# Performance work log

Measured on AMD Instinct MI355X. Metric: run time of the kernel, lower is better.

The kernel has to match this reference:

```python
import jax, jax.numpy as jnp
import numpy as np

USR_NUM = 100000
D_IN = 32
D_HID = 32
D_MID = 16
D_OUT = 2
N_EDGES = 1600000
EPS = 1e-16  # matches torch_geometric.utils.softmax denominator eps


def _glorot(key, shape):
    fan_in, fan_out = shape[0], shape[1]
    lim = np.sqrt(6.0 / (fan_in + fan_out))
    return jax.random.uniform(key, shape, jnp.float32, -lim, lim)


def setup_inputs() -> dict:
    key = jax.random.key(0)
    ks = jax.random.split(key, 16)
    inp = {
        "edge_index": jax.random.randint(ks[0], (2, N_EDGES), 0, USR_NUM, dtype=jnp.int64)
        if jax.config.jax_enable_x64 else jax.random.randint(ks[0], (2, N_EDGES), 0, USR_NUM).astype(jnp.int32),
        "emb": jax.random.normal(ks[1], (USR_NUM, D_IN), jnp.float32),
        # conv1: TransformerConv(32 -> 32, heads=1)
        "Wq1": _glorot(ks[2], (D_IN, D_HID)), "bq1": jnp.zeros((D_HID,), jnp.float32),
        "Wk1": _glorot(ks[3], (D_IN, D_HID)), "bk1": jnp.zeros((D_HID,), jnp.float32),
        "Wv1": _glorot(ks[4], (D_IN, D_HID)), "bv1": jnp.zeros((D_HID,), jnp.float32),
        "Ws1": _glorot(ks[5], (D_IN, D_HID)), "bs1": jnp.zeros((D_HID,), jnp.float32),
        # conv2: TransformerConv(32 -> 16, heads=1)
        "Wq2": _glorot(ks[6], (D_HID, D_MID)), "bq2": jnp.zeros((D_MID,), jnp.float32),
        "Wk2": _glorot(ks[7], (D_HID, D_MID)), "bk2": jnp.zeros((D_MID,), jnp.float32),
        "Wv2": _glorot(ks[8], (D_HID, D_MID)), "bv2": jnp.zeros((D_MID,), jnp.float32),
        "Ws2": _glorot(ks[9], (D_HID, D_MID)), "bs2": jnp.zeros((D_MID,), jnp.float32),
        # output: Linear(16 -> 2)
        "Wo": _glorot(ks[10], (D_MID, D_OUT)), "bo": jnp.zeros((D_OUT,), jnp.float32),
    }
    return inp


def transformer_conv(x, src, dst, Wq, bq, Wk, bk, Wv, bv, Ws, bs, n_nodes):
    # edge (j=src -> i=dst): alpha_ij = softmax_i( <q_i, k_j> / sqrt(d) )
    d = Wq.shape[1]
    q = (x @ Wq + bq)[dst]          # [E, d]
    k = (x @ Wk + bk)[src]          # [E, d]
    v = (x @ Wv + bv)[src]          # [E, d]
    alpha = jnp.sum(q * k, axis=-1) / jnp.sqrt(jnp.float32(d))  # [E]
    # segment softmax over incoming edges of each destination node
    seg_max = jax.ops.segment_max(alpha, dst, num_segments=n_nodes)  # [N]
    e = jnp.exp(alpha - seg_max[dst])
    seg_sum = jax.ops.segment_sum(e, dst, num_segments=n_nodes)      # [N]
    w = e / (seg_sum[dst] + EPS)
    agg = jax.ops.segment_sum(v * w[:, None], dst, num_segments=n_nodes)  # [N, d]
    return agg + x @ Ws + bs  # root/skip connection (PyG default root_weight=True)


def reference(edge_index, emb,
              Wq1, bq1, Wk1, bk1, Wv1, bv1, Ws1, bs1,
              Wq2, bq2, Wk2, bk2, Wv2, bv2, Ws2, bs2,
              Wo, bo):
    src, dst = edge_index[0], edge_index[1]
    h = transformer_conv(emb, src, dst, Wq1, bq1, Wk1, bk1, Wv1, bv1, Ws1, bs1, USR_NUM)
    h = jax.nn.relu(h)
    h = transformer_conv(h, src, dst, Wq2, bq2, Wk2, bk2, Wv2, bv2, Ws2, bs2, USR_NUM)
    h = jax.nn.relu(h)
    return h @ Wo + bo  # [N, 2]
```

## Files before the change

### kernel.cpp

```cpp
#include <hip/hip_runtime.h>
#include <hip/hip_bf16.h>

typedef __hip_bfloat16 bf16;
typedef unsigned int uint;
typedef unsigned short ushort;

#define N_NODES 100000
#define N_EDGES_C 1600000
#define NSB 196
#define NSBP 200
#define SBCAP 10240
#define RND 2048
#define EPB (RND / 256)
#define NBIN 64
#define G_RAD ((N_EDGES_C + RND - 1) / RND)
#define NHB 392
#define HCAP 5632
#define NSLOT (NHB * 256)
#define NCHUNK 16
#define KEYN (256 * NCHUNK)

__device__ __forceinline__ float ldf(const void* p, long i, int isbf) {
    return isbf ? __bfloat162float(((const bf16*)p)[i]) : ((const float*)p)[i];
}
__device__ __forceinline__ int ldidx(const int* ei, long pos, int is64) {
    return is64 ? ei[2 * pos] : ei[pos];
}
__device__ __forceinline__ ushort bfb(float x) {
    bf16 h = __float2bfloat16(x);
    return *(ushort*)&h;
}
__device__ __forceinline__ float bl(uint u) { return __uint_as_float(u << 16); }
__device__ __forceinline__ float bh(uint u) { return __uint_as_float(u & 0xFFFF0000u); }

__global__ void setup_kernel(
    const void* emb, const int* ei,
    const void* Wq1, const void* bq1, const void* Wk1, const void* bk1,
    const void* Wv1, const void* bv1, const void* Ws1, const void* bs1,
    const void* Wq2, const void* bq2, const void* Wk2, const void* bk2,
    const void* Wv2, const void* bv2, const void* Ws2, const void* bs2,
    const void* Wo, const void* bo,
    int* flags, float* wp1, float* bp1, float* wp2, float* bp2, float* woF,
    int* curSB) {
    __shared__ int sf0;
    int t = threadIdx.x;
    if (t < 64) {
        const bf16* pb = (const bf16*)emb;
        int bad = 0;
        for (int i = t; i < 256; i += 64) {
            float v = __bfloat162float(pb[i]);
            if (!(v > -1.0e6f && v < 1.0e6f)) bad++;
        }
        int nz = 0;
        for (int i = 2 * t + 1; i < 256; i += 128) nz += (ei[i] != 0) ? 1 : 0;
#pragma unroll
        for (int m = 32; m >= 1; m >>= 1) {
            bad += __shfl_xor(bad, m, 64);
            nz  += __shfl_xor(nz, m, 64);
        }
        if (t == 0) {
            int f0 = (bad <= 8) ? 1 : 0;
            flags[0] = f0;
            flags[1] = (nz == 0) ? 1 : 0;
            sf0 = f0;
        }
    }
    __syncthreads();
    int isbf = sf0;
    for (int i = t; i < 1024; i += 256) {
        wp1[i]        = ldf(Wq1, i, isbf);
        wp1[1024 + i] = ldf(Wk1, i, isbf);
        wp1[2048 + i] = ldf(Wv1, i, isbf);
        wp1[3072 + i] = ldf(Ws1, i, isbf);
    }
    for (int i = t; i < 512; i += 256) {
        wp2[i]        = ldf(Wq2, i, isbf);
        wp2[512 + i]  = ldf(Wk2, i, isbf);
        wp2[1024 + i] = ldf(Wv2, i, isbf);
        wp2[1536 + i] = ldf(Ws2, i, isbf);
    }
    if (t < 32) {
        bp1[t] = ldf(bq1, t, isbf); bp1[32 + t] = ldf(bk1, t, isbf);
        bp1[64 + t] = ldf(bv1, t, isbf); bp1[96 + t] = ldf(bs1, t, isbf);
        woF[t] = ldf(Wo, t, isbf);
    }
    if (t < 16) {
        bp2[t] = ldf(bq2, t, isbf); bp2[16 + t] = ldf(bk2, t, isbf);
        bp2[32 + t] = ldf(bv2, t, isbf); bp2[48 + t] = ldf(bs2, t, isbf);
    }
    if (t < 2) woF[32 + t] = ldf(bo, t, isbf);
    curSB[t] = 0;
}

template <int DOUT, bool RUNTIME_DTYPE>
__device__ __forceinline__ void node_linear_body(
    const void* __restrict__ X, const float* __restrict__ wpack,
    const float* __restrict__ bpack, const int* __restrict__ flags,
    float* __restrict__ q, ushort* __restrict__ kvb, float* __restrict__ s,
    int bid, float* __restrict__ sW, float* __restrict__ sbias, float* __restrict__ sX) {
    const int TPN = DOUT / 4;
    const int NPB = 256 / TPN;
    const int W_ELEMS = 4 * 32 * DOUT;

    const float4* wp4 = (const float4*)wpack;
    float4* sW4 = (float4*)sW;
    for (int i = threadIdx.x; i < W_ELEMS / 4; i += 256) sW4[i] = wp4[i];
    if (threadIdx.x < 4 * DOUT) sbias[threadIdx.x] = bpack[threadIdx.x];
    const int base = bid * NPB * 32;
    bool useBf = RUNTIME_DTYPE && (flags[0] != 0);
    if (useBf) {
        for (int i = threadIdx.x; i < NPB * 32; i += 256) {
            int g = base + i;
            float xv = (g < N_NODES * 32) ? __bfloat162float(((const bf16*)X)[g]) : 0.0f;
            sX[(i >> 5) * 36 + (i & 31)] = xv;
        }
    } else {
        for (int i = threadIdx.x; i < NPB * 32; i += 256) {
            int g = base + i;
            sX[(i >> 5) * 36 + (i & 31)] = (g < N_NODES * 32) ? ((const float*)X)[g] : 0.0f;
        }
    }
    __syncthreads();

    int l = threadIdx.x / TPN;
    int c4 = (threadIdx.x % TPN) * 4;
    int n = bid * NPB + l;
    if (n >= N_NODES) return;

    float xr[32];
#pragma unroll
    for (int j = 0; j < 8; j++) {
        float4 t4 = *(const float4*)&sX[l * 36 + 4 * j];
        xr[4 * j] = t4.x; xr[4 * j + 1] = t4.y; xr[4 * j + 2] = t4.z; xr[4 * j + 3] = t4.w;
    }
    float acc[4][4];
#pragma unroll
    for (int m = 0; m < 4; m++)
#pragma unroll
        for (int j = 0; j < 4; j++) acc[m][j] = sbias[m * DOUT + c4 + j];

#pragma unroll
    for (int t = 0; t < 32; t++) {
#pragma unroll
        for (int m = 0; m < 4; m++) {
            float4 w = *(const float4*)&sW[(m * 32 + t) * DOUT + c4];
            acc[m][0] += xr[t] * w.x;
            acc[m][1] += xr[t] * w.y;
            acc[m][2] += xr[t] * w.z;
            acc[m][3] += xr[t] * w.w;
        }
    }
    size_t o = (size_t)n * DOUT + c4;
    *(float4*)&q[o] = make_float4(acc[0][0], acc[0][1], acc[0][2], acc[0][3]);
    *(float4*)&s[o] = make_float4(acc[3][0], acc[3][1], acc[3][2], acc[3][3]);
    size_t okv = (size_t)n * 2 * DOUT + c4;
    ushort4 kp = make_ushort4(bfb(acc[1][0]), bfb(acc[1][1]), bfb(acc[1][2]), bfb(acc[1][3]));
    ushort4 vp = make_ushort4(bfb(acc[2][0]), bfb(acc[2][1]), bfb(acc[2][2]), bfb(acc[2][3]));
    *(ushort4*)&kvb[okv]        = kp;
    *(ushort4*)&kvb[okv + DOUT] = vp;
}

struct RadixS {
    int cnt[256]; int excl[256]; int gbase[NSBP];
    uint sVal[RND]; unsigned char sSb[RND];
};
struct LinS { float sW[4096]; float sbias[128]; float sX[32 * 36]; };
union alignas(16) FusedS { RadixS r; LinS l; };

__global__ void __launch_bounds__(256, 4) fused_ra_nl(
    const int* __restrict__ ei, const int* __restrict__ flags,
    int* __restrict__ curSB, uint* __restrict__ pairsSB,
    const void* __restrict__ X, const float* __restrict__ wpack,
    const float* __restrict__ bpack,
    float* __restrict__ q, ushort* __restrict__ kvb, float* __restrict__ s) {
    __shared__ FusedS u;
    if (blockIdx.x >= G_RAD) {
        node_linear_body<32, true>(X, wpack, bpack, flags, q, kvb, s,
                                   (int)blockIdx.x - G_RAD, u.l.sW, u.l.sbias, u.l.sX);
        return;
    }
    int* cnt = u.r.cnt; int* excl = u.r.excl; int* gbase = u.r.gbase;
    uint* sVal = u.r.sVal; unsigned char* sSb = u.r.sSb;
    const int is64 = flags[1];
    int t = threadIdx.x;
    cnt[t] = 0;
    __syncthreads();
    long base = (long)blockIdx.x * RND;

    int mySb[EPB]; int myRank[EPB]; uint myPk[EPB];
#pragma unroll
    for (int r = 0; r < EPB; r++) {
        long e = base + r * 256 + t;
        mySb[r] = -1;
        if (e < N_EDGES_C) {
            int d = ldidx(ei, (long)N_EDGES_C + e, is64);
            int src = ldidx(ei, e, is64);
            int sb = d >> 9;
            myPk[r] = (uint)src | ((uint)(d & 511) << 17);
            myRank[r] = atomicAdd(&cnt[sb], 1);
            mySb[r] = sb;
        }
    }
    __syncthreads();
    int v = cnt[t];
    excl[t] = v;
    __syncthreads();
    for (int off = 1; off < 256; off <<= 1) {
        int u2 = (t >= off) ? excl[t - off] : 0;
        __syncthreads();
        excl[t] += u2;
        __syncthreads();
    }
    int myExcl = excl[t] - v;
    __syncthreads();
    excl[t] = myExcl;
    __syncthreads();
#pragma unroll
    for (int r = 0; r < EPB; r++) {
        if (mySb[r] >= 0) {
            int pos = excl[mySb[r]] + myRank[r];
            sVal[pos] = myPk[r];
            sSb[pos] = (unsigned char)mySb[r];
        }
    }
    __syncthreads();
    if (t < NSBP)
        gbase[t] = (cnt[t] > 0) ? atomicAdd(&curSB[t], cnt[t]) : 0;
    __syncthreads();
    int tot = excl[NSBP - 1] + cnt[NSBP - 1];
    for (int i = t; i < tot; i += 256) {
        int sb = sSb[i];
        int gp = gbase[sb] + (i - excl[sb]);
        if (gp < SBCAP)
            pairsSB[(size_t)sb * SBCAP + gp] = sVal[i];
    }
}

__global__ void __launch_bounds__(256, 2) radix_b(
    const int* __restrict__ curSB, const uint* __restrict__ pairsSB,
    int* __restrict__ esrc,
    int* __restrict__ rowbeg, int* __restrict__ rowend,
    int* __restrict__ perm) {
    __shared__ uint sP[HCAP];
    __shared__ int dcnt[KEYN];
    __shared__ int dexcl[KEYN];
    __shared__ int dcur[KEYN];
    __shared__ int part[256];
    __shared__ int hbin[NBIN], hbase[NBIN], hcur[NBIN];
    __shared__ int scnt;
    int sbh = blockIdx.x;
    int parent = sbh >> 1, half = sbh & 1;
    int t = threadIdx.x;
    int n = min(curSB[parent], SBCAP);
    for (int i = t; i < KEYN; i += 256) { dcnt[i] = 0; dcur[i] = 0; }
    if (t < NBIN) { hbin[t] = 0; hcur[t] = 0; }
    if (t == 0) scnt = 0;
    perm[sbh * 256 + t] = -1;
    __syncthreads();
    const uint* srcp = pairsSB + (size_t)parent * SBCAP;
    for (int i = t; i < n; i += 256) {
        uint pk = srcp[i];
        if (((pk >> 25) & 1u) == (uint)half) {
            int m = atomicAdd(&scnt, 1);
            if (m < HCAP) sP[m] = pk;
            int key = (int)((pk >> 17) & 255) * NCHUNK + (int)((pk & 0x1FFFFu) >> 13);
            atomicAdd(&dcnt[key], 1);
        }
    }
    __syncthreads();
    int nc = min(scnt, HCAP);
    const int kb = t * NCHUNK;
    int sum = 0;
#pragma unroll
    for (int j = 0; j < NCHUNK; j++) sum += dcnt[kb + j];
    int v = sum;
    part[t] = v;
    __syncthreads();
    for (int off = 1; off < 256; off <<= 1) {
        int u2 = (t >= off) ? part[t - off] : 0;
        __syncthreads();
        part[t] += u2;
        __syncthreads();
    }
    int run = part[t] - v;
    int myExcl = run;
#pragma unroll
    for (int j = 0; j < NCHUNK; j++) { dexcl[kb + j] = run; run += dcnt[kb + j]; }
    __syncthreads();
    const int EB = sbh * HCAP;
    int dst = sbh * 256 + t;
    int mybin = -1;
    if (dst < N_NODES) {
        rowbeg[dst] = EB + min(myExcl, HCAP);
        rowend[dst] = EB + min(myExcl + v, HCAP);
        mybin = min(v, NBIN - 1);
        atomicAdd(&hbin[mybin], 1);
    }
    __syncthreads();
    if (t < 64) {
        int hv = hbin[t];
        int sfx = hv;
#pragma unroll
        for (int off = 1; off < 64; off <<= 1) {
            int u2 = __shfl_down(sfx, off, 64);
            if (t + off < 64) sfx += u2;
        }
        hbase[t] = sfx - hv;
    }
    __syncthreads();
    if (dst < N_NODES) {
        int r = atomicAdd(&hcur[mybin], 1);
        perm[sbh * 256 + hbase[mybin] + r] = dst;
    }
    for (int i = t; i < nc; i += 256) {
        uint pk = sP[i];
        int key = (int)((pk >> 17) & 255) * NCHUNK + (int)((pk & 0x1FFFFu) >> 13);
        int p2 = dexcl[key] + atomicAdd(&dcur[key], 1);
        if (p2 < HCAP) esrc[EB + p2] = (int)(pk & 0x1FFFF);
    }
}

template <int D, bool LAYER2>
__global__ void gather_attn(const int* __restrict__ perm,
                            const int* __restrict__ rowbeg, const int* __restrict__ rowend,
                            const int* __restrict__ esrc,
                            const float* __restrict__ q, const ushort* __restrict__ kvb,
                            const float* __restrict__ s,
                            const float* __restrict__ wp2,
                            const float* __restrict__ bp2,
                            const float* __restrict__ woF,
                            const int* __restrict__ flags,
                            float* __restrict__ q2o, ushort* __restrict__ kvb2o,
                            float* __restrict__ s2o,
                            void* __restrict__ out) {
    const int LPD = D / 8;
    const int G = 64 / LPD;
    __shared__ float sW2[2048];
    __shared__ float sb2[64];
    __shared__ float sH[64 * 36];
    __shared__ int sDst[64];

    if constexpr (!LAYER2) {
        for (int i = threadIdx.x; i < 2048; i += 256) sW2[i] = wp2[i];
        if (threadIdx.x < 64) sb2[threadIdx.x] = bp2[threadIdx.x];
    }

    int lane = threadIdx.x & 63;
    int wave = (blockIdx.x * blockDim.x + threadIdx.x) >> 6;
    int g = lane / LPD;
    int c = lane % LPD;
    int idx = wave * G + g;
    if constexpr (LAYER2) {
        if (idx >= NSLOT) return;
    }
    int dst = perm[idx];
    if constexpr (LAYER2) {
        if (dst < 0) return;
    }
    bool alive = (dst >= 0);

    const float rsq = (D == 32) ? 0.17677669529663689f : 0.25f;
    float4 qa = make_float4(0.f, 0.f, 0.f, 0.f), qb = qa;
    int beg = 0, end = 0;
    if (alive) {
        qa = *(const float4*)(q + (size_t)dst * D + 8 * c);
        qb = *(const float4*)(q + (size_t)dst * D + 8 * c + 4);
        beg = rowbeg[dst]; end = rowend[dst];
    }

    const char* kvbase = (const char*)kvb;
    const int ROW = 4 * D;
    const int koff = 16 * c;
    const int voff = 2 * D + 16 * c;

    float sum0 = 0.f, sum1 = 0.f;
    float a0[8] = {0,0,0,0,0,0,0,0};
    float a1[8] = {0,0,0,0,0,0,0,0};

    uint4 kq[4], vq[4];
#pragma unroll
    for (int r = 0; r < 4; r++) {
        int sn = (beg + r < end) ? esrc[beg + r] : 0;
        const char* p = kvbase + (size_t)sn * ROW;
        kq[r] = *(const uint4*)(p + koff);
        vq[r] = *(const uint4*)(p + voff);
    }

    for (int e = beg; e < end; e += 4) {
        uint4 kc[4], vc[4];
#pragma unroll
        for (int r = 0; r < 4; r++) { kc[r] = kq[r]; vc[r] = vq[r]; }
#pragma unroll
        for (int r = 0; r < 4; r++) {
            if (e + 4 + r < end) {
                const char* p = kvbase + (size_t)esrc[e + 4 + r] * ROW;
                kq[r] = *(const uint4*)(p + koff);
                vq[r] = *(const uint4*)(p + voff);
            }
        }
#pragma unroll
        for (int r = 0; r < 4; r++) {
            if (e + r < end) {
                uint4 kA = kc[r], vA = vc[r];
                float pd = qa.x * bl(kA.x) + qa.y * bh(kA.x) + qa.z * bl(kA.y) + qa.w * bh(kA.y)
                         + qb.x * bl(kA.z) + qb.y * bh(kA.z) + qb.z * bl(kA.w) + qb.w * bh(kA.w);
#pragma unroll
                for (int m = LPD / 2; m >= 1; m >>= 1) pd += __shfl_xor(pd, m, LPD);
                float ex = __expf(fminf(fmaxf(pd * rsq, -80.0f), 80.0f));
                if (r & 1) {
                    sum1 += ex;
                    a1[0] += bl(vA.x) * ex; a1[1] += bh(vA.x) * ex;
                    a1[2] += bl(vA.y) * ex; a1[3] += bh(vA.y) * ex;
                    a1[4] += bl(vA.z) * ex; a1[5] += bh(vA.z) * ex;
                    a1[6] += bl(vA.w) * ex; a1[7] += bh(vA.w) * ex;
                } else {
                    sum0 += ex;
                    a0[0] += bl(vA.x) * ex; a0[1] += bh(vA.x) * ex;
                    a0[2] += bl(vA.y) * ex; a0[3] += bh(vA.y) * ex;
                    a0[4] += bl(vA.z) * ex; a0[5] += bh(vA.z) * ex;
                    a0[6] += bl(vA.w) * ex; a0[7] += bh(vA.w) * ex;
                }
            }
        }
    }
    float inv = 1.0f / (sum0 + sum1 + 1e-16f);
    float4 sa = make_float4(0.f, 0.f, 0.f, 0.f), sbv = sa;
    if (alive) {
        sa  = *(const float4*)(s + (size_t)dst * D + 8 * c);
        sbv = *(const float4*)(s + (size_t)dst * D + 8 * c + 4);
    }
    float h[8];
    h[0] = (a0[0] + a1[0]) * inv + sa.x;  h[1] = (a0[1] + a1[1]) * inv + sa.y;
    h[2] = (a0[2] + a1[2]) * inv + sa.z;  h[3] = (a0[3] + a1[3]) * inv + sa.w;
    h[4] = (a0[4] + a1[4]) * inv + sbv.x; h[5] = (a0[5] + a1[5]) * inv + sbv.y;
    h[6] = (a0[6] + a1[6]) * inv + sbv.z; h[7] = (a0[7] + a1[7]) * inv + sbv.w;
#pragma unroll
    for (int j = 0; j < 8; j++) h[j] = h[j] > 0.0f ? h[j] : 0.0f;

    if constexpr (!LAYER2) {
        int gl = (threadIdx.x >> 6) * G + g;
        if (alive) {
            *(float4*)&sH[gl * 36 + 8 * c]     = make_float4(h[0], h[1], h[2], h[3]);
            *(float4*)&sH[gl * 36 + 8 * c + 4] = make_float4(h[4], h[5], h[6], h[7]);
        }
        if (c == 0) sDst[gl] = dst;
        __syncthreads();
        int l = threadIdx.x >> 2;
        int c4 = (threadIdx.x & 3) * 4;
        int nd = sDst[l];
        if (nd >= 0) {
            float acc2[4][4];
#pragma unroll
            for (int m = 0; m < 4; m++)
#pragma unroll
                for (int j = 0; j < 4; j++) acc2[m][j] = sb2[m * 16 + c4 + j];
#pragma unroll
            for (int t2 = 0; t2 < 32; t2++) {
                float xv = sH[l * 36 + t2];
#pragma unroll
                for (int m = 0; m < 4; m++) {
                    float4 w = *(const float4*)&sW2[(m * 32 + t2) * 16 + c4];
                    acc2[m][0] += xv * w.x;
                    acc2[m][1] += xv * w.y;
                    acc2[m][2] += xv * w.z;
                    acc2[m][3] += xv * w.w;
                }
            }
            size_t o = (size_t)nd * 16 + c4;
            *(float4*)&q2o[o] = make_float4(acc2[0][0], acc2[0][1], acc2[0][2], acc2[0][3]);
            *(float4*)&s2o[o] = make_float4(acc2[3][0], acc2[3][1], acc2[3][2], acc2[3][3]);
            size_t okv = (size_t)nd * 32 + c4;
            ushort4 kp = make_ushort4(bfb(acc2[1][0]), bfb(acc2[1][1]), bfb(acc2[1][2]), bfb(acc2[1][3]));
            ushort4 vp = make_ushort4(bfb(acc2[2][0]), bfb(acc2[2][1]), bfb(acc2[2][2]), bfb(acc2[2][3]));
            *(ushort4*)&kvb2o[okv]      = kp;
            *(ushort4*)&kvb2o[okv + 16] = vp;
        }
    } else {
        float p0 = 0.f, p1 = 0.f;
#pragma unroll
        for (int j = 0; j < 8; j++) {
            p0 += h[j] * woF[(8 * c + j) * 2 + 0];
            p1 += h[j] * woF[(8 * c + j) * 2 + 1];
        }
#pragma unroll
        for (int m = LPD / 2; m >= 1; m >>= 1) {
            p0 += __shfl_xor(p0, m, LPD);
            p1 += __shfl_xor(p1, m, LPD);
        }
        if (c == 0) {
            float o0 = p0 + woF[32];
            float o1 = p1 + woF[33];
            if (flags[0]) {
                ((bf16*)out)[dst * 2 + 0] = __float2bfloat16(o0);
                ((bf16*)out)[dst * 2 + 1] = __float2bfloat16(o1);
            } else {
                ((float*)out)[dst * 2 + 0] = o0;
                ((float*)out)[dst * 2 + 1] = o1;
            }
        }
    }
}

extern "C" void kernel_launch(void* const* d_in, const int* in_sizes, int n_in,
                              void* d_out, int out_size, void* d_ws, size_t ws_size,
                              hipStream_t stream) {
    const int* ei  = (const int*)d_in[0];
    const void* emb = d_in[1];
    const void *Wq1 = d_in[2],  *bq1 = d_in[3];
    const void *Wk1 = d_in[4],  *bk1 = d_in[5];
    const void *Wv1 = d_in[6],  *bv1 = d_in[7];
    const void *Ws1 = d_in[8],  *bs1 = d_in[9];
    const void *Wq2 = d_in[10], *bq2 = d_in[11];
    const void *Wk2 = d_in[12], *bk2 = d_in[13];
    const void *Wv2 = d_in[14], *bv2 = d_in[15];
    const void *Ws2 = d_in[16], *bs2 = d_in[17];
    const void *Wo  = d_in[18], *bo  = d_in[19];

    const size_t ND   = (size_t)N_NODES * 32;
    const size_t ND16 = (size_t)N_NODES * 16;
    const size_t SBTOT = (size_t)NSB * SBCAP;
    const size_t ESRC_TOT = (size_t)NHB * HCAP;
    float* base   = (float*)d_ws;
    int*   flags  = (int*)base;
    float* wp1    = base + 64;
    float* bp1    = wp1 + 4096;
    float* wp2    = bp1 + 128;
    float* bp2    = wp2 + 2048;
    float* woF    = bp2 + 64;
    int*   curSB  = (int*)(woF + 64);
    int*   rowbeg = curSB + 256;
    int*   rowend = rowbeg + N_NODES;
    int*   perm   = rowend + N_NODES;
    float* p      = (float*)(perm + NSLOT);
    float* q      = p; p += ND;
    float* s      = p; p += ND;
    ushort* kvb   = (ushort*)p; p += ND;
    float* q2     = p; p += ND16;
    float* s2     = p; p += ND16;
    ushort* kvb2  = (ushort*)p; p += ND16;
    int*   esrc   = (int*)p; p += ESRC_TOT;
    uint*  pairsSB = (uint*)p;

    const int B = 256;
    const int gNL32  = (N_NODES + 31) / 32;
    const int gFused = G_RAD + gNL32;
    const int gG1    = NSLOT / 64;
    const int gG2    = NSLOT / 128;

    setup_kernel<<<1, B, 0, stream>>>(emb, ei,
        Wq1, bq1, Wk1, bk1, Wv1, bv1, Ws1, bs1,
        Wq2, bq2, Wk2, bk2, Wv2, bv2, Ws2, bs2, Wo, bo,
        flags, wp1, bp1, wp2, bp2, woF, curSB);

    fused_ra_nl<<<gFused, B, 0, stream>>>(ei, flags, curSB, pairsSB,
                                          emb, wp1, bp1, q, kvb, s);

    radix_b<<<NHB, B, 0, stream>>>(curSB, pairsSB, esrc, rowbeg, rowend, perm);

    gather_attn<32, false><<<gG1, B, 0, stream>>>(
        perm, rowbeg, rowend, esrc, q, kvb, s, wp2, bp2, nullptr, flags,
        q2, kvb2, s2, nullptr);

    gather_attn<16, true><<<gG2, B, 0, stream>>>(
        perm, rowbeg, rowend, esrc, q2, kvb2, s2, nullptr, nullptr, woF, flags,
        nullptr, nullptr, nullptr, d_out);
}
```

Baseline: 265.0 us.

## Bucket edges directly into 256-node superbuckets and permute gather wave order

Result: no change. 260.7 us (-1.6%).

```diff
diff --git a/kernel.cpp b/kernel.cpp
--- a/kernel.cpp
+++ b/kernel.cpp
@@ -7,16 +7,14 @@
 
 #define N_NODES 100000
 #define N_EDGES_C 1600000
-#define NSB 196
-#define NSBP 200
-#define SBCAP 10240
+#define NSB2 392
+#define NSB2P 512
 #define RND 2048
 #define EPB (RND / 256)
 #define NBIN 64
 #define G_RAD ((N_EDGES_C + RND - 1) / RND)
-#define NHB 392
 #define HCAP 5632
-#define NSLOT (NHB * 256)
+#define NSLOT (NSB2 * 256)
 #define NCHUNK 16
 #define KEYN (256 * NCHUNK)
 
@@ -89,7 +87,7 @@
         bp2[32 + t] = ldf(bv2, t, isbf); bp2[48 + t] = ldf(bs2, t, isbf);
     }
     if (t < 2) woF[32 + t] = ldf(bo, t, isbf);
-    curSB[t] = 0;
+    curSB[t] = 0; curSB[t + 256] = 0;
 }
 
 template <int DOUT, bool RUNTIME_DTYPE>
@@ -161,8 +159,8 @@
 }
 
 struct RadixS {
-    int cnt[256]; int excl[256]; int gbase[NSBP];
-    uint sVal[RND]; unsigned char sSb[RND];
+    int cnt[NSB2P]; int excl[NSB2P]; int part[256]; int gbase[NSB2P];
+    uint sVal[RND]; ushort sSb[RND];
 };
 struct LinS { float sW[4096]; float sbias[128]; float sX[32 * 36]; };
 union alignas(16) FusedS { RadixS r; LinS l; };
@@ -179,11 +177,11 @@
                                    (int)blockIdx.x - G_RAD, u.l.sW, u.l.sbias, u.l.sX);
         return;
     }
-    int* cnt = u.r.cnt; int* excl = u.r.excl; int* gbase = u.r.gbase;
-    uint* sVal = u.r.sVal; unsigned char* sSb = u.r.sSb;
+    int* cnt = u.r.cnt; int* excl = u.r.excl; int* part = u.r.part; int* gbase = u.r.gbase;
+    uint* sVal = u.r.sVal; ushort* sSb = u.r.sSb;
     const int is64 = flags[1];
     int t = threadIdx.x;
-    cnt[t] = 0;
+    cnt[t] = 0; cnt[t + 256] = 0;
     __syncthreads();
     long base = (long)blockIdx.x * RND;
 
@@ -195,44 +193,44 @@
         if (e < N_EDGES_C) {
             int d = ldidx(ei, (long)N_EDGES_C + e, is64);
             int src = ldidx(ei, e, is64);
-            int sb = d >> 9;
-            myPk[r] = (uint)src | ((uint)(d & 511) << 17);
+            int sb = d >> 8;
+            myPk[r] = (uint)src | ((uint)(d & 255) << 17);
             myRank[r] = atomicAdd(&cnt[sb], 1);
             mySb[r] = sb;
         }
     }
     __syncthreads();
-    int v = cnt[t];
-    excl[t] = v;
+    int v0 = cnt[2 * t], v1 = cnt[2 * t + 1];
+    int sum2 = v0 + v1;
+    part[t] = sum2;
     __syncthreads();
     for (int off = 1; off < 256; off <<= 1) {
-        int u2 = (t >= off) ? excl[t - off] : 0;
+        int u2 = (t >= off) ? part[t - off] : 0;
         __syncthreads();
-        excl[t] += u2;
+        part[t] += u2;
         __syncthreads();
     }
-    int myExcl = excl[t] - v;
-    __syncthreads();
-    excl[t] = myExcl;
+    int basex = part[t] - sum2;
+    excl[2 * t]     = basex;
+    excl[2 * t + 1] = basex + v0;
     __syncthreads();
 #pragma unroll
     for (int r = 0; r < EPB; r++) {
         if (mySb[r] >= 0) {
             int pos = excl[mySb[r]] + myRank[r];
             sVal[pos] = myPk[r];
-            sSb[pos] = (unsigned char)mySb[r];
-        }
-    }
-    __syncthreads();
-    if (t < NSBP)
-        gbase[t] = (cnt[t] > 0) ? atomicAdd(&curSB[t], cnt[t]) : 0;
-    __syncthreads();
-    int tot = excl[NSBP - 1] + cnt[NSBP - 1];
+            sSb[pos] = (ushort)mySb[r];
+        }
+    }
+    for (int i = t; i < NSB2P; i += 256)
+        gbase[i] = (cnt[i] > 0) ? atomicAdd(&curSB[i], cnt[i]) : 0;
+    __syncthreads();
+    int tot = excl[NSB2P - 1] + cnt[NSB2P - 1];
     for (int i = t; i < tot; i += 256) {
         int sb = sSb[i];
         int gp = gbase[sb] + (i - excl[sb]);
-        if (gp < SBCAP)
-            pairsSB[(size_t)sb * SBCAP + gp] = sVal[i];
+        if (gp < HCAP)
+            pairsSB[(size_t)sb * HCAP + gp] = sVal[i];
     }
 }
 
@@ -247,28 +245,21 @@
     __shared__ int dcur[KEYN];
     __shared__ int part[256];
     __shared__ int hbin[NBIN], hbase[NBIN], hcur[NBIN];
-    __shared__ int scnt;
     int sbh = blockIdx.x;
-    int parent = sbh >> 1, half = sbh & 1;
     int t = threadIdx.x;
-    int n = min(curSB[parent], SBCAP);
+    int n = min(curSB[sbh], HCAP);
     for (int i = t; i < KEYN; i += 256) { dcnt[i] = 0; dcur[i] = 0; }
     if (t < NBIN) { hbin[t] = 0; hcur[t] = 0; }
-    if (t == 0) scnt = 0;
     perm[sbh * 256 + t] = -1;
     __syncthreads();
-    const uint* srcp = pairsSB + (size_t)parent * SBCAP;
+    const uint* srcp = pairsSB + (size_t)sbh * HCAP;
     for (int i = t; i < n; i += 256) {
         uint pk = srcp[i];
-        if (((pk >> 25) & 1u) == (uint)half) {
-            int m = atomicAdd(&scnt, 1);
-            if (m < HCAP) sP[m] = pk;
-            int key = (int)((pk >> 17) & 255) * NCHUNK + (int)((pk & 0x1FFFFu) >> 13);
-            atomicAdd(&dcnt[key], 1);
-        }
-    }
-    __syncthreads();
-    int nc = min(scnt, HCAP);
+        sP[i] = pk;
+        int key = (int)((pk >> 17) & 255) * NCHUNK + (int)((pk & 0x1FFFFu) >> 13);
+        atomicAdd(&dcnt[key], 1);
+    }
+    __syncthreads();
     const int kb = t * NCHUNK;
     int sum = 0;
 #pragma unroll
@@ -312,7 +303,7 @@
         int r = atomicAdd(&hcur[mybin], 1);
         perm[sbh * 256 + hbase[mybin] + r] = dst;
     }
-    for (int i = t; i < nc; i += 256) {
+    for (int i = t; i < n; i += 256) {
         uint pk = sP[i];
         int key = (int)((pk >> 17) & 255) * NCHUNK + (int)((pk & 0x1FFFFu) >> 13);
         int p2 = dexcl[key] + atomicAdd(&dcur[key], 1);
@@ -335,6 +326,7 @@
                             void* __restrict__ out) {
     const int LPD = D / 8;
     const int G = 64 / LPD;
+    const int WPC = 256 / G;
     __shared__ float sW2[2048];
     __shared__ float sb2[64];
     __shared__ float sH[64 * 36];
@@ -346,13 +338,12 @@
     }
 
     int lane = threadIdx.x & 63;
-    int wave = (blockIdx.x * blockDim.x + threadIdx.x) >> 6;
+    int W = (blockIdx.x * blockDim.x + threadIdx.x) >> 6;
     int g = lane / LPD;
     int c = lane % LPD;
-    int idx = wave * G + g;
-    if constexpr (LAYER2) {
-        if (idx >= NSLOT) return;
-    }
+    int chunkc = W / WPC;
+    int window = ((W % WPC) * 5) % WPC;
+    int idx = chunkc * 256 + window * G + g;
     int dst = perm[idx];
     if constexpr (LAYER2) {
         if (dst < 0) return;
@@ -518,8 +509,7 @@
 
     const size_t ND   = (size_t)N_NODES * 32;
     const size_t ND16 = (size_t)N_NODES * 16;
-    const size_t SBTOT = (size_t)NSB * SBCAP;
-    const size_t ESRC_TOT = (size_t)NHB * HCAP;
+    const size_t SBTOT = (size_t)NSB2 * HCAP;
     float* base   = (float*)d_ws;
     int*   flags  = (int*)base;
     float* wp1    = base + 64;
@@ -528,7 +518,7 @@
     float* bp2    = wp2 + 2048;
     float* woF    = bp2 + 64;
     int*   curSB  = (int*)(woF + 64);
-    int*   rowbeg = curSB + 256;
+    int*   rowbeg = curSB + 512;
     int*   rowend = rowbeg + N_NODES;
     int*   perm   = rowend + N_NODES;
     float* p      = (float*)(perm + NSLOT);
@@ -538,7 +528,7 @@
     float* q2     = p; p += ND16;
     float* s2     = p; p += ND16;
     ushort* kvb2  = (ushort*)p; p += ND16;
-    int*   esrc   = (int*)p; p += ESRC_TOT;
+    int*   esrc   = (int*)p; p += SBTOT;
     uint*  pairsSB = (uint*)p;
 
     const int B = 256;
@@ -555,7 +545,7 @@
     fused_ra_nl<<<gFused, B, 0, stream>>>(ei, flags, curSB, pairsSB,
                                           emb, wp1, bp1, q, kvb, s);
 
-    radix_b<<<NHB, B, 0, stream>>>(curSB, pairsSB, esrc, rowbeg, rowend, perm);
+    radix_b<<<NSB2, B, 0, stream>>>(curSB, pairsSB, esrc, rowbeg, rowend, perm);
 
     gather_attn<32, false><<<gG1, B, 0, stream>>>(
         perm, rowbeg, rowend, esrc, q, kvb, s, wp2, bp2, nullptr, flags,
```
